# Performance work log

Measured on AMD Instinct MI355X. Metric: run time of the kernel, lower is better.

Reference implementation:

```python
import jax, jax.numpy as jnp
import numpy as np

N = 100000   # nodes
E = 1600000  # edges
F_IN = 256   # input features
H = 64       # hidden
C = 40       # classes


def setup_inputs() -> dict:
    key = jax.random.key(0)
    k = jax.random.split(key, 5)
    x = jax.random.normal(k[0], (N, F_IN), dtype=jnp.float32)
    edge_index = jax.random.randint(k[1], (2, E), 0, N, dtype=jnp.int64)
    edge_attr = jax.random.uniform(k[2], (E,), dtype=jnp.float32)
    # GCNConv params (glorot-ish scale), biases zero like reset_parameters
    W1 = jax.random.normal(k[3], (F_IN, H), dtype=jnp.float32) * (1.0 / np.sqrt(F_IN))
    b1 = jnp.zeros((H,), dtype=jnp.float32)
    W2 = jax.random.normal(k[4], (H, C), dtype=jnp.float32) * (1.0 / np.sqrt(H))
    b2 = jnp.zeros((C,), dtype=jnp.float32)
    return {"x": x, "edge_index": edge_index, "edge_attr": edge_attr,
            "W1": W1, "b1": b1, "W2": W2, "b2": b2}


def _gcn_conv(x, W, b, src, dst, norm):
    h = x @ W                                   # [N, out]
    msg = h[src] * norm[:, None]                # gather + edge scale [E+N, out]
    out = jax.ops.segment_sum(msg, dst, num_segments=N)
    return out + b


def reference(x, edge_index, edge_attr, W1, b1, W2, b2):
    # gcn_norm: add self-loops (weight 1), symmetric D^-1/2 A D^-1/2
    loop = jnp.arange(N, dtype=edge_index.dtype)
    src = jnp.concatenate([edge_index[0], loop])
    dst = jnp.concatenate([edge_index[1], loop])
    w = jnp.concatenate([edge_attr, jnp.ones((N,), dtype=edge_attr.dtype)])
    deg = jax.ops.segment_sum(w, dst, num_segments=N)
    dinv = jnp.where(deg > 0, jax.lax.rsqrt(jnp.maximum(deg, 1e-30)), 0.0)
    norm = dinv[src] * w * dinv[dst]

    h = _gcn_conv(x, W1, b1, src, dst, norm)
    h = jax.nn.relu(h)                          # dropout is identity in eval mode
    h = _gcn_conv(h, W2, b2, src, dst, norm)
    return jax.nn.log_softmax(h, axis=1)
```

## Files before the change

kernel.cpp:

```cpp
#include <hip/hip_runtime.h>
#include <math.h>

#define NN   100000
#define NE   1600000
#define FIN  256
#define HID  64
#define NC   40
#define NBKT 391
#define EPB  6250
#define CAP  4608
#define NT   6250

typedef __attribute__((ext_vector_type(8))) short short8;
typedef __attribute__((ext_vector_type(4))) float float4v;

static __device__ __forceinline__ short f2bf(float f) {
    unsigned u = __float_as_uint(f);
    u += 0x7FFFu + ((u >> 16) & 1u);
    return (short)(u >> 16);
}
static __device__ __forceinline__ float bf2f(unsigned short b) {
    return __uint_as_float((unsigned)b << 16);
}

__global__ __launch_bounds__(256) void w1cvt_k(const float* __restrict__ W1,
                                               short* __restrict__ w1t) {
    int t = blockIdx.x * 256 + threadIdx.x;
    int k = t >> 6, n = t & 63;
    w1t[n * FIN + k] = f2bf(W1[k * HID + n]);
}

__global__ __launch_bounds__(256) void phaseA_k(const int* __restrict__ src,
                                                const int* __restrict__ dst,
                                                const float* __restrict__ w,
                                                int* __restrict__ cursor,
                                                int2* __restrict__ bucketbuf) {
    __shared__ int  hist[NBKT];
    __shared__ int  sc[512];
    __shared__ int  loc_base[NBKT];
    __shared__ int  loc_cur[NBKT];
    __shared__ int  gb[NBKT];
    __shared__ int2 buf[EPB];
    const int t  = threadIdx.x;
    const int e0 = blockIdx.x * EPB;

    for (int i = t; i < NBKT; i += 256) hist[i] = 0;
    __syncthreads();
    for (int i = t; i < EPB; i += 256) atomicAdd(&hist[dst[e0 + i] >> 8], 1);
    __syncthreads();
    sc[t]       = (t       < NBKT) ? hist[t]       : 0;
    sc[t + 256] = (t + 256 < NBKT) ? hist[t + 256] : 0;
    __syncthreads();
    for (int off = 1; off < 512; off <<= 1) {
        int a0 = (t >= off) ? sc[t - off] : 0;
        int a1 = sc[t + 256 - off];
        __syncthreads();
        sc[t] += a0; sc[t + 256] += a1;
        __syncthreads();
    }
    for (int i = t; i < NBKT; i += 256) {
        int base = sc[i] - hist[i];
        loc_base[i] = base;
        loc_cur[i]  = base;
        gb[i] = atomicAdd(&cursor[i * 16], hist[i]);
    }
    __syncthreads();
    for (int i = t; i < EPB; i += 256) {
        int e = e0 + i;
        int d = dst[e];
        int b = d >> 8;
        int p = atomicAdd(&loc_cur[b], 1);
        buf[p] = make_int2(src[e] | ((d & 255) << 17), __float_as_int(w[e]));
    }
    __syncthreads();
    for (int b = t; b < NBKT; b += 256) {
        int lb = loc_base[b], n = hist[b];
        int2* dstp = bucketbuf + (size_t)b * CAP + gb[b];
        for (int i = 0; i < n; ++i) dstp[i] = buf[lb + i];
    }
}

__global__ __launch_bounds__(512) void scanB_k(const int* __restrict__ cursor,
                                               int* __restrict__ bucketbase,
                                               int* __restrict__ row_start) {
    __shared__ int tmp[512];
    int t = threadIdx.x;
    int v = (t < NBKT) ? cursor[t * 16] : 0;
    tmp[t] = v;
    __syncthreads();
    for (int off = 1; off < 512; off <<= 1) {
        int add = (t >= off) ? tmp[t - off] : 0;
        __syncthreads(); tmp[t] += add; __syncthreads();
    }
    if (t < NBKT) bucketbase[t] = tmp[t] - v;
    if (t == 0) { bucketbase[NBKT] = NE; row_start[NN] = NE; }
}

__global__ __launch_bounds__(256) void phaseB_k(const int* __restrict__ bucketbase,
                                                const int2* __restrict__ bucketbuf,
                                                int2* __restrict__ e8,
                                                int* __restrict__ row_start,
                                                float* __restrict__ dinv) {
    __shared__ int2 buf[CAP];
    __shared__ int2 buf2[CAP];
    __shared__ int  hist2[256];
    __shared__ int  tmp[256];
    __shared__ int  base2[257];
    __shared__ int  cur2[256];
    const int b = blockIdx.x, t = threadIdx.x;
    const int g0   = bucketbase[b];
    const int cntb = bucketbase[b + 1] - g0;
    const int n0   = b * 256;
    const int nnb  = (NN - n0 < 256) ? (NN - n0) : 256;

    hist2[t] = 0;
    __syncthreads();
    const int2* bb = bucketbuf + (size_t)b * CAP;
    for (int i = t; i < cntb; i += 256) {
        int2 kv = bb[i];
        buf[i] = kv;
        atomicAdd(&hist2[kv.x >> 17], 1);
    }
    __syncthreads();
    int v = hist2[t];
    tmp[t] = v;
    __syncthreads();
    for (int off = 1; off < 256; off <<= 1) {
        int add = (t >= off) ? tmp[t - off] : 0;
        __syncthreads(); tmp[t] += add; __syncthreads();
    }
    int excl = tmp[t] - v;
    base2[t] = excl;
    cur2[t]  = excl;
    if (t == 0) base2[256] = cntb;
    if (t < nnb) row_start[n0 + t] = g0 + excl;
    __syncthreads();
    for (int i = t; i < cntb; i += 256) {
        int2 kv = buf[i];
        int d = kv.x >> 17;
        int p = atomicAdd(&cur2[d], 1);
        buf2[p] = make_int2(kv.x & 0x1FFFF, kv.y);
    }
    __syncthreads();
    for (int i = t; i < cntb; i += 256) e8[g0 + i] = buf2[i];
    if (t < nnb) {
        float s = 0.f;
        int j1 = base2[t + 1];
        for (int j = base2[t]; j < j1; ++j) s += __int_as_float(buf2[j].y);
        dinv[n0 + t] = rsqrtf(1.0f + s);
    }
}

__global__ __launch_bounds__(256) void e8scale_k(int2* __restrict__ e8,
                                                 const float* __restrict__ dinv) {
    int e = blockIdx.x * 256 + threadIdx.x;
    int2 kv = e8[e];
    kv.y = __float_as_int(__int_as_float(kv.y) * dinv[kv.x]);
    e8[e] = kv;
}

static __device__ __forceinline__ void stage_tile(const float* __restrict__ x, int t,
                                                  float* buf, int lane) {
#pragma unroll
    for (int j = 0; j < 16; ++j) {
        const float* gsrc = x + (size_t)t * (16 * FIN) + j * FIN + ((lane ^ (j & 7)) << 2);
        __builtin_amdgcn_global_load_lds(
            (const __attribute__((address_space(1))) void*)gsrc,
            (__attribute__((address_space(3))) void*)(buf + j * 256), 16, 0, 0);
    }
}

__global__ __launch_bounds__(256, 1) void gemm1_mfma_k(const float* __restrict__ x,
                                                       const short* __restrict__ w1t,
                                                       unsigned short* __restrict__ h1) {
    __shared__ float xs[4 * 2 * 16 * 256];
    const int wave = threadIdx.x >> 6;
    const int lane = threadIdx.x & 63;
    const int m    = lane & 15;
    const int quad = lane >> 4;
    const int wid  = blockIdx.x * 4 + wave;

    short8 bf[4][8];
#pragma unroll
    for (int nb = 0; nb < 4; ++nb)
#pragma unroll
        for (int kc = 0; kc < 8; ++kc)
            bf[nb][kc] = *(const short8*)(w1t + (nb * 16 + m) * FIN + kc * 32 + quad * 8);

    float* buf0 = xs + (wave * 2) * (16 * 256);
    float* buf1 = buf0 + 16 * 256;
    const unsigned sw = (unsigned)(m & 7) << 4;

    int t = wid, cur = 0;
    if (t < NT) stage_tile(x, t, buf0, lane);
    for (; t < NT; t += 1024) {
        int tn = t + 1024;
        float* bcur  = cur ? buf1 : buf0;
        float* bnext = cur ? buf0 : buf1;
        if (tn < NT) {
            stage_tile(x, tn, bnext, lane);
            asm volatile("s_waitcnt vmcnt(16)" ::: "memory");
        } else {
            asm volatile("s_waitcnt vmcnt(0)" ::: "memory");
        }
        __builtin_amdgcn_sched_barrier(0);

        const char* xrow = (const char*)(bcur + m * 256);
        float4v acc0 = {0.f,0.f,0.f,0.f}, acc1 = acc0, acc2 = acc0, acc3 = acc0;
#pragma unroll
        for (int kc = 0; kc < 8; ++kc) {
            const unsigned c0 = (unsigned)(kc * 128 + quad * 32);
            float4v xa = *(const float4v*)(xrow + (c0 ^ sw));
            float4v xb = *(const float4v*)(xrow + ((c0 + 16) ^ sw));
            short8 a;
            a[0] = f2bf(xa[0]); a[1] = f2bf(xa[1]); a[2] = f2bf(xa[2]); a[3] = f2bf(xa[3]);
            a[4] = f2bf(xb[0]); a[5] = f2bf(xb[1]); a[6] = f2bf(xb[2]); a[7] = f2bf(xb[3]);
            acc0 = __builtin_amdgcn_mfma_f32_16x16x32_bf16(a, bf[0][kc], acc0, 0, 0, 0);
            acc1 = __builtin_amdgcn_mfma_f32_16x16x32_bf16(a, bf[1][kc], acc1, 0, 0, 0);
            acc2 = __builtin_amdgcn_mfma_f32_16x16x32_bf16(a, bf[2][kc], acc2, 0, 0, 0);
            acc3 = __builtin_amdgcn_mfma_f32_16x16x32_bf16(a, bf[3][kc], acc3, 0, 0, 0);
        }
#pragma unroll
        for (int r = 0; r < 4; ++r) {
            int rr = t * 16 + quad * 4 + r;
            unsigned short* hp = h1 + (size_t)rr * HID + m;
            hp[0]  = (unsigned short)f2bf(acc0[r]);
            hp[16] = (unsigned short)f2bf(acc1[r]);
            hp[32] = (unsigned short)f2bf(acc2[r]);
            hp[48] = (unsigned short)f2bf(acc3[r]);
        }
        cur ^= 1;
    }
}

__global__ __launch_bounds__(256) void gatherA_k(const int* __restrict__ row_start,
                                                 const int2* __restrict__ e8,
                                                 const float* __restrict__ dinv,
                                                 const unsigned short* __restrict__ h,
                                                 const float* __restrict__ b1,
                                                 unsigned short* __restrict__ Rp) {
    const int v    = blockIdx.x * 4 + (threadIdx.x >> 6);
    const int lane = threadIdx.x & 63;
    const int slot = lane >> 3;
    const int fg   = lane & 7;
    const int i0 = row_start[v], i1 = row_start[v + 1];

    float acc[8] = {0.f,0.f,0.f,0.f,0.f,0.f,0.f,0.f};
    for (int i = i0; i < i1; i += 16) {
        int iiA = i + slot, iiB = i + 8 + slot;
        bool okA = iiA < i1, okB = iiB < i1;
        int2 eA = e8[okA ? iiA : (NE - 1)];
        int2 eB = e8[okB ? iiB : (NE - 1)];
        int  sA = okA ? eA.x : 0;
        int  sB = okB ? eB.x : 0;
        float wA = okA ? __int_as_float(eA.y) : 0.f;
        float wB = okB ? __int_as_float(eB.y) : 0.f;
        uint4 pA = *(const uint4*)(h + (size_t)sA * HID + fg * 8);
        uint4 pB = *(const uint4*)(h + (size_t)sB * HID + fg * 8);
        acc[0] = fmaf(__uint_as_float(pA.x << 16),         wA, acc[0]);
        acc[1] = fmaf(__uint_as_float(pA.x & 0xFFFF0000u), wA, acc[1]);
        acc[2] = fmaf(__uint_as_float(pA.y << 16),         wA, acc[2]);
        acc[3] = fmaf(__uint_as_float(pA.y & 0xFFFF0000u), wA, acc[3]);
        acc[4] = fmaf(__uint_as_float(pA.z << 16),         wA, acc[4]);
        acc[5] = fmaf(__uint_as_float(pA.z & 0xFFFF0000u), wA, acc[5]);
        acc[6] = fmaf(__uint_as_float(pA.w << 16),         wA, acc[6]);
        acc[7] = fmaf(__uint_as_float(pA.w & 0xFFFF0000u), wA, acc[7]);
        acc[0] = fmaf(__uint_as_float(pB.x << 16),         wB, acc[0]);
        acc[1] = fmaf(__uint_as_float(pB.x & 0xFFFF0000u), wB, acc[1]);
        acc[2] = fmaf(__uint_as_float(pB.y << 16),         wB, acc[2]);
        acc[3] = fmaf(__uint_as_float(pB.y & 0xFFFF0000u), wB, acc[3]);
        acc[4] = fmaf(__uint_as_float(pB.z << 16),         wB, acc[4]);
        acc[5] = fmaf(__uint_as_float(pB.z & 0xFFFF0000u), wB, acc[5]);
        acc[6] = fmaf(__uint_as_float(pB.w << 16),         wB, acc[6]);
        acc[7] = fmaf(__uint_as_float(pB.w & 0xFFFF0000u), wB, acc[7]);
    }
#pragma unroll
    for (int mk = 8; mk <= 32; mk <<= 1) {
#pragma unroll
        for (int q = 0; q < 8; ++q) acc[q] += __shfl_xor(acc[q], mk);
    }

    const float dv  = dinv[v];
    const float dv2 = dv * dv;
    uint4 ps = *(const uint4*)(h + (size_t)v * HID + fg * 8);
    float4 bA = *(const float4*)(b1 + fg * 8);
    float4 bB = *(const float4*)(b1 + fg * 8 + 4);
    float r0 = fmaxf(dv * acc[0] + dv2 * __uint_as_float(ps.x << 16)         + bA.x, 0.f);
    float r1 = fmaxf(dv * acc[1] + dv2 * __uint_as_float(ps.x & 0xFFFF0000u) + bA.y, 0.f);
    float r2 = fmaxf(dv * acc[2] + dv2 * __uint_as_float(ps.y << 16)         + bA.z, 0.f);
    float r3 = fmaxf(dv * acc[3] + dv2 * __uint_as_float(ps.y & 0xFFFF0000u) + bA.w, 0.f);
    float r4 = fmaxf(dv * acc[4] + dv2 * __uint_as_float(ps.z << 16)         + bB.x, 0.f);
    float r5 = fmaxf(dv * acc[5] + dv2 * __uint_as_float(ps.z & 0xFFFF0000u) + bB.y, 0.f);
    float r6 = fmaxf(dv * acc[6] + dv2 * __uint_as_float(ps.w << 16)         + bB.z, 0.f);
    float r7 = fmaxf(dv * acc[7] + dv2 * __uint_as_float(ps.w & 0xFFFF0000u) + bB.w, 0.f);
    if (slot == 0) {
        uint4 pk;
        pk.x = (unsigned)(unsigned short)f2bf(r0) | ((unsigned)(unsigned short)f2bf(r1) << 16);
        pk.y = (unsigned)(unsigned short)f2bf(r2) | ((unsigned)(unsigned short)f2bf(r3) << 16);
        pk.z = (unsigned)(unsigned short)f2bf(r4) | ((unsigned)(unsigned short)f2bf(r5) << 16);
        pk.w = (unsigned)(unsigned short)f2bf(r6) | ((unsigned)(unsigned short)f2bf(r7) << 16);
        *(uint4*)(Rp + (size_t)v * HID + fg * 8) = pk;
    }
}

__global__ __launch_bounds__(256) void gatherB_k(const int* __restrict__ row_start,
                                                 const int2* __restrict__ e8,
                                                 const float* __restrict__ dinv,
                                                 const unsigned short* __restrict__ Rp,
                                                 float* __restrict__ agg2) {
    const int v    = blockIdx.x * 4 + (threadIdx.x >> 6);
    const int lane = threadIdx.x & 63;
    const int slot = lane >> 3;
    const int fg   = lane & 7;
    const int i0 = row_start[v], i1 = row_start[v + 1];

    float acc[8] = {0.f,0.f,0.f,0.f,0.f,0.f,0.f,0.f};
    for (int i = i0; i < i1; i += 16) {
        int iiA = i + slot, iiB = i + 8 + slot;
        bool okA = iiA < i1, okB = iiB < i1;
        int2 eA = e8[okA ? iiA : (NE - 1)];
        int2 eB = e8[okB ? iiB : (NE - 1)];
        int  sA = okA ? eA.x : 0;
        int  sB = okB ? eB.x : 0;
        float wA = okA ? __int_as_float(eA.y) : 0.f;
        float wB = okB ? __int_as_float(eB.y) : 0.f;
        uint4 pA = *(const uint4*)(Rp + (size_t)sA * HID + fg * 8);
        uint4 pB = *(const uint4*)(Rp + (size_t)sB * HID + fg * 8);
        acc[0] = fmaf(__uint_as_float(pA.x << 16),         wA, acc[0]);
        acc[1] = fmaf(__uint_as_float(pA.x & 0xFFFF0000u), wA, acc[1]);
        acc[2] = fmaf(__uint_as_float(pA.y << 16),         wA, acc[2]);
        acc[3] = fmaf(__uint_as_float(pA.y & 0xFFFF0000u), wA, acc[3]);
        acc[4] = fmaf(__uint_as_float(pA.z << 16),         wA, acc[4]);
        acc[5] = fmaf(__uint_as_float(pA.z & 0xFFFF0000u), wA, acc[5]);
        acc[6] = fmaf(__uint_as_float(pA.w << 16),         wA, acc[6]);
        acc[7] = fmaf(__uint_as_float(pA.w & 0xFFFF0000u), wA, acc[7]);
        acc[0] = fmaf(__uint_as_float(pB.x << 16),         wB, acc[0]);
        acc[1] = fmaf(__uint_as_float(pB.x & 0xFFFF0000u), wB, acc[1]);
        acc[2] = fmaf(__uint_as_float(pB.y << 16),         wB, acc[2]);
        acc[3] = fmaf(__uint_as_float(pB.y & 0xFFFF0000u), wB, acc[3]);
        acc[4] = fmaf(__uint_as_float(pB.z << 16),         wB, acc[4]);
        acc[5] = fmaf(__uint_as_float(pB.z & 0xFFFF0000u), wB, acc[5]);
        acc[6] = fmaf(__uint_as_float(pB.w << 16),         wB, acc[6]);
        acc[7] = fmaf(__uint_as_float(pB.w & 0xFFFF0000u), wB, acc[7]);
    }
#pragma unroll
    for (int mk = 8; mk <= 32; mk <<= 1) {
#pragma unroll
        for (int q = 0; q < 8; ++q) acc[q] += __shfl_xor(acc[q], mk);
    }

    const float dv  = dinv[v];
    const float dv2 = dv * dv;
    uint4 ps = *(const uint4*)(Rp + (size_t)v * HID + fg * 8);
    if (slot == 0) {
        float4 oA, oB;
        oA.x = dv * acc[0] + dv2 * __uint_as_float(ps.x << 16);
        oA.y = dv * acc[1] + dv2 * __uint_as_float(ps.x & 0xFFFF0000u);
        oA.z = dv * acc[2] + dv2 * __uint_as_float(ps.y << 16);
        oA.w = dv * acc[3] + dv2 * __uint_as_float(ps.y & 0xFFFF0000u);
        oB.x = dv * acc[4] + dv2 * __uint_as_float(ps.z << 16);
        oB.y = dv * acc[5] + dv2 * __uint_as_float(ps.z & 0xFFFF0000u);
        oB.z = dv * acc[6] + dv2 * __uint_as_float(ps.w << 16);
        oB.w = dv * acc[7] + dv2 * __uint_as_float(ps.w & 0xFFFF0000u);
        *(float4*)(agg2 + (size_t)v * HID + fg * 8)     = oA;
        *(float4*)(agg2 + (size_t)v * HID + fg * 8 + 4) = oB;
    }
}

__global__ __launch_bounds__(256) void gemm3_logsm_k(const float* __restrict__ agg2,
                                                     const float* __restrict__ W2,
                                                     const float* __restrict__ b2,
                                                     float* __restrict__ out) {
    __shared__ float w2s[HID * NC];
    __shared__ float b2s[NC];
    for (int i = threadIdx.x; i < HID * NC; i += 256) w2s[i] = W2[i];
    if (threadIdx.x < NC) b2s[threadIdx.x] = b2[threadIdx.x];
    __syncthreads();

    const int r = blockIdx.x * 256 + threadIdx.x;
    if (r >= NN) return;
    float acc[NC];
#pragma unroll
    for (int c = 0; c < NC; ++c) acc[c] = b2s[c];

    const float4* row4 = (const float4*)(agg2 + (size_t)r * HID);
    for (int kk = 0; kk < HID; kk += 4) {
        float4 v = row4[kk >> 2];
#pragma unroll
        for (int c = 0; c < NC; ++c) {
            acc[c] = fmaf(v.x, w2s[(kk + 0) * NC + c], acc[c]);
            acc[c] = fmaf(v.y, w2s[(kk + 1) * NC + c], acc[c]);
            acc[c] = fmaf(v.z, w2s[(kk + 2) * NC + c], acc[c]);
            acc[c] = fmaf(v.w, w2s[(kk + 3) * NC + c], acc[c]);
        }
    }
    float m = acc[0];
#pragma unroll
    for (int c = 1; c < NC; ++c) m = fmaxf(m, acc[c]);
    float s = 0.f;
#pragma unroll
    for (int c = 0; c < NC; ++c) s += __expf(acc[c] - m);
    float lg = m + __logf(s);
    float* outp = out + (size_t)r * NC;
#pragma unroll
    for (int c = 0; c < NC; c += 4)
        *(float4*)&outp[c] = make_float4(acc[c] - lg, acc[c+1] - lg, acc[c+2] - lg, acc[c+3] - lg);
}

extern "C" void kernel_launch(void* const* d_in, const int* in_sizes, int n_in,
                              void* d_out, int out_size, void* d_ws, size_t ws_size,
                              hipStream_t stream) {
    const float* x  = (const float*)d_in[0];
    const int*   ei = (const int*)d_in[1];
    const float* ea = (const float*)d_in[2];
    const float* W1 = (const float*)d_in[3];
    const float* b1 = (const float*)d_in[4];
    const float* W2 = (const float*)d_in[5];
    const float* b2 = (const float*)d_in[6];
    const int* src = ei;
    const int* dst = ei + NE;
    float* out = (float*)d_out;

    char* ws = (char*)d_ws;
    float* dinv       = (float*)(ws + 0);
    int*   row_start  = (int*)  (ws + 400000);
    int*   cursor     = (int*)  (ws + 800016);
    int*   bucketbase = (int*)  (ws + 825040);
    int2*  e8         = (int2*) (ws + 826608);
    unsigned short* h1 = (unsigned short*)(ws + 13626608);
    unsigned short* Rp = (unsigned short*)(ws + 26426608);
    float* agg2       = (float*)(ws + 39226608);
    short* w1t        = (short*)(ws + 64826608);
    int2*  bucketbuf  = (int2*)agg2;

    hipMemsetAsync(cursor, 0, 391 * 16 * sizeof(int), stream);

    w1cvt_k <<<64,   256, 0, stream>>>(W1, w1t);
    phaseA_k<<<256,  256, 0, stream>>>(src, dst, ea, cursor, bucketbuf);
    scanB_k <<<1,    512, 0, stream>>>(cursor, bucketbase, row_start);
    phaseB_k<<<NBKT, 256, 0, stream>>>(bucketbase, bucketbuf, e8, row_start, dinv);
    e8scale_k<<<NE / 256, 256, 0, stream>>>(e8, dinv);

    gemm1_mfma_k <<<256,  256, 0, stream>>>(x, w1t, h1);
    gatherA_k    <<<NN / 4, 256, 0, stream>>>(row_start, e8, dinv, h1, b1, Rp);
    gatherB_k    <<<NN / 4, 256, 0, stream>>>(row_start, e8, dinv, Rp, agg2);
    gemm3_logsm_k<<<(NN + 255) / 256, 256, 0, stream>>>(agg2, W2, b2, out);
}
```

Before: 378.1 us.

## Fuse second-layer GEMM and log-softmax into gather; split GEMM1 staging into halves

The second aggregation kernel now applies W2, adds b2 and computes log-softmax in-wave with shuffles, so the intermediate agg2 buffer and the separate gemm3 kernel are gone. GEMM1 halves its per-wave LDS buffer by staging each 16-row tile in two K-halves, overlapping the load of one half with compute on the other. It also doubles the grid and drops the occupancy-1 launch bound. The fused epilogue reads W2 from global per lane, and the finer-grained pipeline adds more wait points.

```diff
diff --git a/kernel.cpp b/kernel.cpp
--- a/kernel.cpp
+++ b/kernel.cpp
@@ -10,6 +10,7 @@
 #define EPB  6250
 #define CAP  4608
 #define NT   6250
+#define NWV  2048
 
 typedef __attribute__((ext_vector_type(8))) short short8;
 typedef __attribute__((ext_vector_type(4))) float float4v;
@@ -159,21 +160,23 @@
     e8[e] = kv;
 }
 
-static __device__ __forceinline__ void stage_tile(const float* __restrict__ x, int t,
+static __device__ __forceinline__ void stage_half(const float* __restrict__ x, int t, int h,
                                                   float* buf, int lane) {
 #pragma unroll
-    for (int j = 0; j < 16; ++j) {
-        const float* gsrc = x + (size_t)t * (16 * FIN) + j * FIN + ((lane ^ (j & 7)) << 2);
+    for (int j = 0; j < 8; ++j) {
+        int row = 2 * j + (lane >> 5);
+        int c   = (lane & 31) ^ (row & 7);
+        const float* gsrc = x + ((size_t)t * 16 + row) * FIN + h * 128 + c * 4;
         __builtin_amdgcn_global_load_lds(
             (const __attribute__((address_space(1))) void*)gsrc,
             (__attribute__((address_space(3))) void*)(buf + j * 256), 16, 0, 0);
     }
 }
 
-__global__ __launch_bounds__(256, 1) void gemm1_mfma_k(const float* __restrict__ x,
-                                                       const short* __restrict__ w1t,
-                                                       unsigned short* __restrict__ h1) {
-    __shared__ float xs[4 * 2 * 16 * 256];
+__global__ __launch_bounds__(256) void gemm1_mfma_k(const float* __restrict__ x,
+                                                    const short* __restrict__ w1t,
+                                                    unsigned short* __restrict__ h1) {
+    __shared__ float xs[4 * 2 * 2048];
     const int wave = threadIdx.x >> 6;
     const int lane = threadIdx.x & 63;
     const int m    = lane & 15;
@@ -187,39 +190,48 @@
         for (int kc = 0; kc < 8; ++kc)
             bf[nb][kc] = *(const short8*)(w1t + (nb * 16 + m) * FIN + kc * 32 + quad * 8);
 
-    float* buf0 = xs + (wave * 2) * (16 * 256);
-    float* buf1 = buf0 + 16 * 256;
+    float* bufA = xs + wave * 4096;
+    float* bufB = bufA + 2048;
     const unsigned sw = (unsigned)(m & 7) << 4;
 
-    int t = wid, cur = 0;
-    if (t < NT) stage_tile(x, t, buf0, lane);
-    for (; t < NT; t += 1024) {
-        int tn = t + 1024;
-        float* bcur  = cur ? buf1 : buf0;
-        float* bnext = cur ? buf0 : buf1;
+#define COMPUTE_HALF(bufh, kbase)                                                        \
+    {                                                                                    \
+        const char* xrow = (const char*)(bufh) + m * 512;                                \
+        _Pragma("unroll")                                                                \
+        for (int kcl = 0; kcl < 4; ++kcl) {                                              \
+            const unsigned c0 = (unsigned)(kcl * 128 + quad * 32);                       \
+            float4v xa = *(const float4v*)(xrow + (c0 ^ sw));                            \
+            float4v xb = *(const float4v*)(xrow + ((c0 + 16) ^ sw));                     \
+            short8 a;                                                                    \
+            a[0]=f2bf(xa[0]); a[1]=f2bf(xa[1]); a[2]=f2bf(xa[2]); a[3]=f2bf(xa[3]);      \
+            a[4]=f2bf(xb[0]); a[5]=f2bf(xb[1]); a[6]=f2bf(xb[2]); a[7]=f2bf(xb[3]);      \
+            acc0 = __builtin_amdgcn_mfma_f32_16x16x32_bf16(a, bf[0][(kbase)+kcl], acc0, 0, 0, 0); \
+            acc1 = __builtin_amdgcn_mfma_f32_16x16x32_bf16(a, bf[1][(kbase)+kcl], acc1, 0, 0, 0); \
+            acc2 = __builtin_amdgcn_mfma_f32_16x16x32_bf16(a, bf[2][(kbase)+kcl], acc2, 0, 0, 0); \
+            acc3 = __builtin_amdgcn_mfma_f32_16x16x32_bf16(a, bf[3][(kbase)+kcl], acc3, 0, 0, 0); \
+        }                                                                                \
+    }
+
+    int t = wid;
+    if (t < NT) stage_half(x, t, 0, bufA, lane);
+    while (t < NT) {
+        stage_half(x, t, 1, bufB, lane);
+        asm volatile("s_waitcnt vmcnt(8)" ::: "memory");
+        __builtin_amdgcn_sched_barrier(0);
+        float4v acc0 = {0.f,0.f,0.f,0.f}, acc1 = acc0, acc2 = acc0, acc3 = acc0;
+        COMPUTE_HALF(bufA, 0);
+        __builtin_amdgcn_sched_barrier(0);
+
+        int tn = t + NWV;
         if (tn < NT) {
-            stage_tile(x, tn, bnext, lane);
-            asm volatile("s_waitcnt vmcnt(16)" ::: "memory");
+            stage_half(x, tn, 0, bufA, lane);
+            asm volatile("s_waitcnt vmcnt(8)" ::: "memory");
         } else {
             asm volatile("s_waitcnt vmcnt(0)" ::: "memory");
         }
         __builtin_amdgcn_sched_barrier(0);
-
-        const char* xrow = (const char*)(bcur + m * 256);
-        float4v acc0 = {0.f,0.f,0.f,0.f}, acc1 = acc0, acc2 = acc0, acc3 = acc0;
-#pragma unroll
-        for (int kc = 0; kc < 8; ++kc) {
-            const unsigned c0 = (unsigned)(kc * 128 + quad * 32);
-            float4v xa = *(const float4v*)(xrow + (c0 ^ sw));
-            float4v xb = *(const float4v*)(xrow + ((c0 + 16) ^ sw));
-            short8 a;
-            a[0] = f2bf(xa[0]); a[1] = f2bf(xa[1]); a[2] = f2bf(xa[2]); a[3] = f2bf(xa[3]);
-            a[4] = f2bf(xb[0]); a[5] = f2bf(xb[1]); a[6] = f2bf(xb[2]); a[7] = f2bf(xb[3]);
-            acc0 = __builtin_amdgcn_mfma_f32_16x16x32_bf16(a, bf[0][kc], acc0, 0, 0, 0);
-            acc1 = __builtin_amdgcn_mfma_f32_16x16x32_bf16(a, bf[1][kc], acc1, 0, 0, 0);
-            acc2 = __builtin_amdgcn_mfma_f32_16x16x32_bf16(a, bf[2][kc], acc2, 0, 0, 0);
-            acc3 = __builtin_amdgcn_mfma_f32_16x16x32_bf16(a, bf[3][kc], acc3, 0, 0, 0);
-        }
+        COMPUTE_HALF(bufB, 4);
+
 #pragma unroll
         for (int r = 0; r < 4; ++r) {
             int rr = t * 16 + quad * 4 + r;
@@ -229,8 +241,9 @@
             hp[32] = (unsigned short)f2bf(acc2[r]);
             hp[48] = (unsigned short)f2bf(acc3[r]);
         }
-        cur ^= 1;
-    }
+        t = tn;
+    }
+#undef COMPUTE_HALF
 }
 
 __global__ __launch_bounds__(256) void gatherA_k(const int* __restrict__ row_start,
@@ -303,11 +316,13 @@
     }
 }
 
-__global__ __launch_bounds__(256) void gatherB_k(const int* __restrict__ row_start,
-                                                 const int2* __restrict__ e8,
-                                                 const float* __restrict__ dinv,
-                                                 const unsigned short* __restrict__ Rp,
-                                                 float* __restrict__ agg2) {
+__global__ __launch_bounds__(256) void gatherBC_k(const int* __restrict__ row_start,
+                                                  const int2* __restrict__ e8,
+                                                  const float* __restrict__ dinv,
+                                                  const unsigned short* __restrict__ Rp,
+                                                  const float* __restrict__ W2,
+                                                  const float* __restrict__ b2,
+                                                  float* __restrict__ out) {
     const int v    = blockIdx.x * 4 + (threadIdx.x >> 6);
     const int lane = threadIdx.x & 63;
     const int slot = lane >> 3;
@@ -352,59 +367,49 @@
     const float dv  = dinv[v];
     const float dv2 = dv * dv;
     uint4 ps = *(const uint4*)(Rp + (size_t)v * HID + fg * 8);
-    if (slot == 0) {
-        float4 oA, oB;
-        oA.x = dv * acc[0] + dv2 * __uint_as_float(ps.x << 16);
-        oA.y = dv * acc[1] + dv2 * __uint_as_float(ps.x & 0xFFFF0000u);
-        oA.z = dv * acc[2] + dv2 * __uint_as_float(ps.y << 16);
-        oA.w = dv * acc[3] + dv2 * __uint_as_float(ps.y & 0xFFFF0000u);
-        oB.x = dv * acc[4] + dv2 * __uint_as_float(ps.z << 16);
-        oB.y = dv * acc[5] + dv2 * __uint_as_float(ps.z & 0xFFFF0000u);
-        oB.z = dv * acc[6] + dv2 * __uint_as_float(ps.w << 16);
-        oB.w = dv * acc[7] + dv2 * __uint_as_float(ps.w & 0xFFFF0000u);
-        *(float4*)(agg2 + (size_t)v * HID + fg * 8)     = oA;
-        *(float4*)(agg2 + (size_t)v * HID + fg * 8 + 4) = oB;
-    }
-}
-
-__global__ __launch_bounds__(256) void gemm3_logsm_k(const float* __restrict__ agg2,
-                                                     const float* __restrict__ W2,
-                                                     const float* __restrict__ b2,
-                                                     float* __restrict__ out) {
-    __shared__ float w2s[HID * NC];
-    __shared__ float b2s[NC];
-    for (int i = threadIdx.x; i < HID * NC; i += 256) w2s[i] = W2[i];
-    if (threadIdx.x < NC) b2s[threadIdx.x] = b2[threadIdx.x];
-    __syncthreads();
-
-    const int r = blockIdx.x * 256 + threadIdx.x;
-    if (r >= NN) return;
-    float acc[NC];
-#pragma unroll
-    for (int c = 0; c < NC; ++c) acc[c] = b2s[c];
-
-    const float4* row4 = (const float4*)(agg2 + (size_t)r * HID);
-    for (int kk = 0; kk < HID; kk += 4) {
-        float4 v = row4[kk >> 2];
-#pragma unroll
-        for (int c = 0; c < NC; ++c) {
-            acc[c] = fmaf(v.x, w2s[(kk + 0) * NC + c], acc[c]);
-            acc[c] = fmaf(v.y, w2s[(kk + 1) * NC + c], acc[c]);
-            acc[c] = fmaf(v.z, w2s[(kk + 2) * NC + c], acc[c]);
-            acc[c] = fmaf(v.w, w2s[(kk + 3) * NC + c], acc[c]);
-        }
-    }
-    float m = acc[0];
-#pragma unroll
-    for (int c = 1; c < NC; ++c) m = fmaxf(m, acc[c]);
-    float s = 0.f;
-#pragma unroll
-    for (int c = 0; c < NC; ++c) s += __expf(acc[c] - m);
-    float lg = m + __logf(s);
-    float* outp = out + (size_t)r * NC;
-#pragma unroll
-    for (int c = 0; c < NC; c += 4)
-        *(float4*)&outp[c] = make_float4(acc[c] - lg, acc[c+1] - lg, acc[c+2] - lg, acc[c+3] - lg);
+    float o[8];
+    o[0] = dv * acc[0] + dv2 * __uint_as_float(ps.x << 16);
+    o[1] = dv * acc[1] + dv2 * __uint_as_float(ps.x & 0xFFFF0000u);
+    o[2] = dv * acc[2] + dv2 * __uint_as_float(ps.y << 16);
+    o[3] = dv * acc[3] + dv2 * __uint_as_float(ps.y & 0xFFFF0000u);
+    o[4] = dv * acc[4] + dv2 * __uint_as_float(ps.z << 16);
+    o[5] = dv * acc[5] + dv2 * __uint_as_float(ps.z & 0xFFFF0000u);
+    o[6] = dv * acc[6] + dv2 * __uint_as_float(ps.w << 16);
+    o[7] = dv * acc[7] + dv2 * __uint_as_float(ps.w & 0xFFFF0000u);
+
+    float p0 = b2[5 * slot + 0], p1 = b2[5 * slot + 1], p2 = b2[5 * slot + 2];
+    float p3 = b2[5 * slot + 3], p4 = b2[5 * slot + 4];
+    const float* wp = W2 + (size_t)(fg * 8) * NC + slot * 5;
+#pragma unroll
+    for (int j = 0; j < 8; ++j) {
+        const float* wr = wp + j * NC;
+        float oj = o[j];
+        p0 = fmaf(oj, wr[0], p0);
+        p1 = fmaf(oj, wr[1], p1);
+        p2 = fmaf(oj, wr[2], p2);
+        p3 = fmaf(oj, wr[3], p3);
+        p4 = fmaf(oj, wr[4], p4);
+    }
+#pragma unroll
+    for (int mk = 1; mk <= 4; mk <<= 1) {
+        p0 += __shfl_xor(p0, mk);
+        p1 += __shfl_xor(p1, mk);
+        p2 += __shfl_xor(p2, mk);
+        p3 += __shfl_xor(p3, mk);
+        p4 += __shfl_xor(p4, mk);
+    }
+    float mx = fmaxf(fmaxf(fmaxf(p0, p1), fmaxf(p2, p3)), p4);
+#pragma unroll
+    for (int mk = 8; mk <= 32; mk <<= 1) mx = fmaxf(mx, __shfl_xor(mx, mk));
+    float e = __expf(p0 - mx) + __expf(p1 - mx) + __expf(p2 - mx)
+            + __expf(p3 - mx) + __expf(p4 - mx);
+#pragma unroll
+    for (int mk = 8; mk <= 32; mk <<= 1) e += __shfl_xor(e, mk);
+    float lg = mx + __logf(e);
+    if (fg == 0) {
+        float* op = out + (size_t)v * NC + slot * 5;
+        op[0] = p0 - lg; op[1] = p1 - lg; op[2] = p2 - lg; op[3] = p3 - lg; op[4] = p4 - lg;
+    }
 }
 
 extern "C" void kernel_launch(void* const* d_in, const int* in_sizes, int n_in,
@@ -429,10 +434,8 @@
     int2*  e8         = (int2*) (ws + 826608);
     unsigned short* h1 = (unsigned short*)(ws + 13626608);
     unsigned short* Rp = (unsigned short*)(ws + 26426608);
-    float* agg2       = (float*)(ws + 39226608);
+    int2*  bucketbuf  = (int2*) (ws + 39226608);
     short* w1t        = (short*)(ws + 64826608);
-    int2*  bucketbuf  = (int2*)agg2;
-
     hipMemsetAsync(cursor, 0, 391 * 16 * sizeof(int), stream);
 
     w1cvt_k <<<64,   256, 0, stream>>>(W1, w1t);
@@ -441,8 +444,7 @@
     phaseB_k<<<NBKT, 256, 0, stream>>>(bucketbase, bucketbuf, e8, row_start, dinv);
     e8scale_k<<<NE / 256, 256, 0, stream>>>(e8, dinv);
 
-    gemm1_mfma_k <<<256,  256, 0, stream>>>(x, w1t, h1);
+    gemm1_mfma_k <<<512,  256, 0, stream>>>(x, w1t, h1);
     gatherA_k    <<<NN / 4, 256, 0, stream>>>(row_start, e8, dinv, h1, b1, Rp);
-    gatherB_k    <<<NN / 4, 256, 0, stream>>>(row_start, e8, dinv, Rp, agg2);
-    gemm3_logsm_k<<<(NN + 255) / 256, 256, 0, stream>>>(agg2, W2, b2, out);
-}
+    gatherBC_k   <<<NN / 4, 256, 0, stream>>>(row_start, e8, dinv, Rp, W2, b2, out);
+}
```

Result: slower. 465.7 us (+23.2%).
